# Optimization experiments

Measured on AMD Instinct MI355X. Metric: run time of the kernel, lower is better.

The kernel has to match this reference:

```python
import jax, jax.numpy as jnp
import numpy as np

N_HEAD = 16

def setup_inputs() -> dict:
    key = jax.random.key(0)
    ks = jax.random.split(key, 5)
    C = 1024
    x = jax.random.normal(ks[0], (2, 2048, C), dtype=jnp.float32)
    w_attn = jax.random.normal(ks[1], (C, 3 * C), dtype=jnp.float32) * (C ** -0.5)
    b_attn = jax.random.normal(ks[2], (3 * C,), dtype=jnp.float32) * 0.02
    w_proj = jax.random.normal(ks[3], (C, C), dtype=jnp.float32) * (C ** -0.5)
    b_proj = jax.random.normal(ks[4], (C,), dtype=jnp.float32) * 0.02
    return {"x": x, "w_attn": w_attn, "b_attn": b_attn, "w_proj": w_proj, "b_proj": b_proj}

def reference(x, w_attn, b_attn, w_proj, b_proj):
    B, T, C = x.shape
    H = N_HEAD
    D = C // H  # head_dim
    qkv = x @ w_attn + b_attn  # [B,T,3C]
    q, k, v = jnp.split(qkv, 3, axis=-1)
    # [B,T,H,D] -> [B,H,T,D]
    q = q.reshape(B, T, H, D).transpose(0, 2, 1, 3)
    k = k.reshape(B, T, H, D).transpose(0, 2, 1, 3)
    v = v.reshape(B, T, H, D).transpose(0, 2, 1, 3)
    scale = 1.0 / np.sqrt(D).astype(np.float32)
    att = jnp.einsum('bhqd,bhkd->bhqk', q, k) * scale  # [B,H,T,T]
    causal = jnp.tril(jnp.ones((T, T), dtype=bool))
    att = jnp.where(causal, att, jnp.finfo(att.dtype).min)
    att = jax.nn.softmax(att, axis=-1)
    y = jnp.einsum('bhqk,bhkd->bhqd', att, v)  # [B,H,T,D]
    y = y.transpose(0, 2, 1, 3).reshape(B, T, C)
    return y @ w_proj + b_proj
```

## Files before the change

kernel.cpp:

```cpp
#include <hip/hip_runtime.h>
#include <hip/hip_bf16.h>
#include <stdint.h>

typedef __bf16 bf16x8 __attribute__((ext_vector_type(8)));
typedef __bf16 bf16x4 __attribute__((ext_vector_type(4)));
typedef float  f32x4  __attribute__((ext_vector_type(4)));

#define GLOBAL_AS __attribute__((address_space(1)))
#define LDS_AS    __attribute__((address_space(3)))

__device__ __forceinline__ void gld_lds16(const __bf16* g, __bf16* l) {
  __builtin_amdgcn_global_load_lds((GLOBAL_AS void*)g, (LDS_AS void*)l, 16, 0, 0);
}

#define QSCALE 0.18033688011116029f

__device__ __forceinline__ unsigned pk2(float a, float b) {
  unsigned short ua = __builtin_bit_cast(unsigned short, (__bf16)a);
  unsigned short ub = __builtin_bit_cast(unsigned short, (__bf16)b);
  return (unsigned)ua | ((unsigned)ub << 16);
}

union PackU { unsigned u[4]; bf16x8 v; };

__global__ __launch_bounds__(256) void cast_bf16_kernel(const float* __restrict__ src,
                                                        __bf16* __restrict__ dst, int n)
{
  int i = (blockIdx.x * 256 + threadIdx.x) * 8;
  if (i >= n) return;
  float4 a = *(const float4*)(src + i);
  float4 b = *(const float4*)(src + i + 4);
  bf16x8 o;
  o[0]=(__bf16)a.x; o[1]=(__bf16)a.y; o[2]=(__bf16)a.z; o[3]=(__bf16)a.w;
  o[4]=(__bf16)b.x; o[5]=(__bf16)b.y; o[6]=(__bf16)b.z; o[7]=(__bf16)b.w;
  *(bf16x8*)(dst + i) = o;
}

__global__ __launch_bounds__(256) void transpose_cast_kernel(const float* __restrict__ src,
                                                             __bf16* __restrict__ dst,
                                                             int R, int C)
{
  __shared__ float tile[32][33];
  int c0 = blockIdx.x * 32, r0 = blockIdx.y * 32;
  int tx = threadIdx.x & 31, ty = threadIdx.x >> 5;
  #pragma unroll
  for (int i = 0; i < 32; i += 8)
    tile[ty + i][tx] = src[(size_t)(r0 + ty + i) * C + (c0 + tx)];
  __syncthreads();
  #pragma unroll
  for (int i = 0; i < 32; i += 8)
    dst[(size_t)(c0 + ty + i) * R + (r0 + tx)] = (__bf16)tile[tx][ty + i];
}

template<int MODE, int BM>
__global__ __launch_bounds__(256, (BM == 128 ? 3 : 2))
void gemm_kernel(const __bf16* __restrict__ A,
                 const __bf16* __restrict__ Bt,
                 const float*  __restrict__ bias,
                 float* __restrict__ outF,
                 __bf16* __restrict__ qb,
                 __bf16* __restrict__ kb,
                 __bf16* __restrict__ vb,
                 int M, int N, int K)
{
  __shared__ __bf16 As[BM * 64];
  __shared__ __bf16 Bs[128 * 64];
  const int tid  = threadIdx.x;
  const int wave = tid >> 6, lane = tid & 63;
  const int lo = lane & 15, g4 = lane >> 4;
  int bm, bn;
  if (MODE == 0) {
    int bid = blockIdx.x;
    int bm_i = (bid & 7) * 4 + ((bid >> 3) & 3);
    int bn_i = bid >> 5;
    bm = bm_i * 128; bn = bn_i * 128;
  } else {
    bm = blockIdx.y * BM; bn = blockIdx.x * 128;
  }
  const int wr = (wave >> 1) * (BM / 2);
  const int wc = (wave & 1) * 64;
  constexpr int MF = BM / 32;

  f32x4 acc[MF][4] = {};

  const int nkt = K >> 6;
  for (int kt = 0; kt < nkt; ++kt) {
    const int k0 = kt << 6;
    __syncthreads();
    #pragma unroll
    for (int j = 0; j < BM / 32; ++j) {
      int c = j * 256 + tid;
      int r = c >> 3, cc = c & 7;
      int cs = cc ^ (r & 7);
      gld_lds16(A + (size_t)(bm + r) * K + (k0 + cs * 8), As + c * 8);
    }
    #pragma unroll
    for (int j = 0; j < 4; ++j) {
      int c = j * 256 + tid;
      int r = c >> 3, cc = c & 7;
      int cs = cc ^ (r & 7);
      gld_lds16(Bt + (size_t)(bn + r) * K + (k0 + cs * 8), Bs + c * 8);
    }
    __syncthreads();
    #pragma unroll
    for (int ks = 0; ks < 2; ++ks) {
      bf16x8 af[MF], bfr[4];
      #pragma unroll
      for (int mf = 0; mf < MF; ++mf) {
        int row = wr + mf * 16 + lo;
        int ch = (ks * 4 + g4) ^ (row & 7);
        af[mf] = *(const bf16x8*)(As + row * 64 + ch * 8);
      }
      #pragma unroll
      for (int nf = 0; nf < 4; ++nf) {
        int row = wc + nf * 16 + lo;
        int ch = (ks * 4 + g4) ^ (row & 7);
        bfr[nf] = *(const bf16x8*)(Bs + row * 64 + ch * 8);
      }
      #pragma unroll
      for (int mf = 0; mf < MF; ++mf)
        #pragma unroll
        for (int nf = 0; nf < 4; ++nf)
          acc[mf][nf] = __builtin_amdgcn_mfma_f32_16x16x32_bf16(af[mf], bfr[nf], acc[mf][nf], 0, 0, 0);
    }
  }

  float bv[4];
  #pragma unroll
  for (int nf = 0; nf < 4; ++nf) bv[nf] = bias[bn + wc + nf * 16 + lo];

  if (MODE == 1) {
    #pragma unroll
    for (int mf = 0; mf < MF; ++mf)
      #pragma unroll
      for (int nf = 0; nf < 4; ++nf) {
        int col = bn + wc + nf * 16 + lo;
        #pragma unroll
        for (int j = 0; j < 4; ++j) {
          int row = bm + wr + mf * 16 + g4 * 4 + j;
          outF[(size_t)row * N + col] = acc[mf][nf][j] + bv[nf];
        }
      }
  } else {
    #pragma unroll
    for (int mf = 0; mf < MF; ++mf) {
      const int tbase = bm + wr + mf * 16 + g4 * 4;
      const int b = tbase >> 11, t = tbase & 2047;
      #pragma unroll
      for (int nf = 0; nf < 4; ++nf) {
        int n = bn + wc + nf * 16 + lo;
        int sel = n >> 10, hd = n & 1023;
        int h = hd >> 6, d = hd & 63;
        size_t bh = (size_t)(b * 16 + h);
        if (sel == 2) {
          bf16x4 pv;
          #pragma unroll
          for (int j = 0; j < 4; ++j) pv[j] = (__bf16)(acc[mf][nf][j] + bv[nf]);
          *(bf16x4*)(vb + (bh * 64 + d) * 2048 + t) = pv;
        } else if (sel == 0) {
          #pragma unroll
          for (int j = 0; j < 4; ++j)
            qb[(bh * 2048 + (size_t)(t + j)) * 64 + d] = (__bf16)((acc[mf][nf][j] + bv[nf]) * QSCALE);
        } else {
          #pragma unroll
          for (int j = 0; j < 4; ++j)
            kb[(bh * 2048 + (size_t)(t + j)) * 64 + d] = (__bf16)(acc[mf][nf][j] + bv[nf]);
        }
      }
    }
  }
}

__global__ __launch_bounds__(256, 4)
void attn_kernel(const __bf16* __restrict__ qg_, const __bf16* __restrict__ kg,
                 const __bf16* __restrict__ vg, __bf16* __restrict__ yg,
                 __bf16* __restrict__ pY, float* __restrict__ pL)
{
  const int n = blockIdx.x;
  const int xcd = n & 7;
  const int m = n >> 3;
  const int bh = xcd + 8 * (m & 3);
  const int t = m >> 2;
  const int b = bh >> 4, h = bh & 15;

  const int tid  = threadIdx.x;
  const int wave = tid >> 6;
  const int lane = tid & 63;
  const int l15  = lane & 15;
  const int g    = lane >> 4;
  const int sw   = l15 & 7;

  __shared__ __bf16 Kb[2][64 * 64];
  __shared__ __bf16 Vb[2][64 * 64];

  const __bf16* qbase = qg_ + (size_t)bh * 2048 * 64;
  const __bf16* kbase = kg  + (size_t)bh * 2048 * 64;
  const __bf16* vbase = vg  + (size_t)bh * 64 * 2048;

  bf16x8 qf0, qf1;
  f32x4 o0, o1, o2, o3, osum;

  bf16x8 ones;
  #pragma unroll
  for (int j = 0; j < 8; ++j) ones[j] = (__bf16)1.0f;

  auto LOADQ = [&](int strip) {
    const int q16 = strip * 64 + wave * 16 + l15;
    qf0 = *(const bf16x8*)(qbase + (size_t)q16 * 64 + g * 8);
    qf1 = *(const bf16x8*)(qbase + (size_t)q16 * 64 + 32 + g * 8);
  };
  auto RESET = [&]() {
    o0 = f32x4{}; o1 = f32x4{}; o2 = f32x4{}; o3 = f32x4{}; osum = f32x4{};
  };
  auto STAGE = [&](int kt, int bsel) {
    #pragma unroll
    for (int j = 0; j < 2; ++j) {
      int c = j * 256 + tid;
      int cr = c >> 3, cc = c & 7;
      int cs = cc ^ (cr & 7);
      int pr = (cr & 0x23) | ((cr & 0x10) >> 2) | ((cr & 0x0C) << 1);
      gld_lds16(kbase + (size_t)(kt * 64 + pr) * 64 + cs * 8, &Kb[bsel][0] + c * 8);
      gld_lds16(vbase + (size_t)cr * 2048 + (kt * 64 + cs * 8), &Vb[bsel][0] + c * 8);
    }
  };

  auto TILE = [&](int cur, bool diag) {
    const __bf16* KL = &Kb[cur][0];
    f32x4 s0 = {}, s1 = {}, s2 = {}, s3 = {};
    {
      bf16x8 k00 = *(const bf16x8*)(KL + (0  + l15) * 64 + ((0 + g) ^ sw) * 8);
      bf16x8 k01 = *(const bf16x8*)(KL + (0  + l15) * 64 + ((4 + g) ^ sw) * 8);
      s0 = __builtin_amdgcn_mfma_f32_16x16x32_bf16(k00, qf0, s0, 0, 0, 0);
      s0 = __builtin_amdgcn_mfma_f32_16x16x32_bf16(k01, qf1, s0, 0, 0, 0);
      bf16x8 k10 = *(const bf16x8*)(KL + (16 + l15) * 64 + ((0 + g) ^ sw) * 8);
      bf16x8 k11 = *(const bf16x8*)(KL + (16 + l15) * 64 + ((4 + g) ^ sw) * 8);
      s1 = __builtin_amdgcn_mfma_f32_16x16x32_bf16(k10, qf0, s1, 0, 0, 0);
      s1 = __builtin_amdgcn_mfma_f32_16x16x32_bf16(k11, qf1, s1, 0, 0, 0);
      bf16x8 k20 = *(const bf16x8*)(KL + (32 + l15) * 64 + ((0 + g) ^ sw) * 8);
      bf16x8 k21 = *(const bf16x8*)(KL + (32 + l15) * 64 + ((4 + g) ^ sw) * 8);
      s2 = __builtin_amdgcn_mfma_f32_16x16x32_bf16(k20, qf0, s2, 0, 0, 0);
      s2 = __builtin_amdgcn_mfma_f32_16x16x32_bf16(k21, qf1, s2, 0, 0, 0);
      bf16x8 k30 = *(const bf16x8*)(KL + (48 + l15) * 64 + ((0 + g) ^ sw) * 8);
      bf16x8 k31 = *(const bf16x8*)(KL + (48 + l15) * 64 + ((4 + g) ^ sw) * 8);
      s3 = __builtin_amdgcn_mfma_f32_16x16x32_bf16(k30, qf0, s3, 0, 0, 0);
      s3 = __builtin_amdgcn_mfma_f32_16x16x32_bf16(k31, qf1, s3, 0, 0, 0);
    }

    if (diag) {
      const int qr = wave * 16 + l15;
      #pragma unroll
      for (int r2 = 0; r2 < 4; ++r2) {
        if (8 * g + r2          > qr) s0[r2] = -3.0e38f;
        if (8 * g + 4 + r2      > qr) s1[r2] = -3.0e38f;
        if (32 + 8 * g + r2     > qr) s2[r2] = -3.0e38f;
        if (32 + 8 * g + 4 + r2 > qr) s3[r2] = -3.0e38f;
      }
    }

    #pragma unroll
    for (int r2 = 0; r2 < 4; ++r2) s0[r2] = exp2f(s0[r2]);
    #pragma unroll
    for (int r2 = 0; r2 < 4; ++r2) s1[r2] = exp2f(s1[r2]);
    #pragma unroll
    for (int r2 = 0; r2 < 4; ++r2) s2[r2] = exp2f(s2[r2]);
    #pragma unroll
    for (int r2 = 0; r2 < 4; ++r2) s3[r2] = exp2f(s3[r2]);

    PackU pa0, pa1;
    pa0.u[0] = pk2(s0[0], s0[1]); pa0.u[1] = pk2(s0[2], s0[3]);
    pa0.u[2] = pk2(s1[0], s1[1]); pa0.u[3] = pk2(s1[2], s1[3]);
    pa1.u[0] = pk2(s2[0], s2[1]); pa1.u[1] = pk2(s2[2], s2[3]);
    pa1.u[2] = pk2(s3[0], s3[1]); pa1.u[3] = pk2(s3[2], s3[3]);

    osum = __builtin_amdgcn_mfma_f32_16x16x32_bf16(pa0.v, ones, osum, 0, 0, 0);
    osum = __builtin_amdgcn_mfma_f32_16x16x32_bf16(pa1.v, ones, osum, 0, 0, 0);

    const __bf16* VL = &Vb[cur][0];
    {
      bf16x8 v00 = *(const bf16x8*)(VL + (0  + l15) * 64 + ((0 + g) ^ sw) * 8);
      bf16x8 v01 = *(const bf16x8*)(VL + (0  + l15) * 64 + ((4 + g) ^ sw) * 8);
      o0 = __builtin_amdgcn_mfma_f32_16x16x32_bf16(pa0.v, v00, o0, 0, 0, 0);
      o0 = __builtin_amdgcn_mfma_f32_16x16x32_bf16(pa1.v, v01, o0, 0, 0, 0);
      bf16x8 v10 = *(const bf16x8*)(VL + (16 + l15) * 64 + ((0 + g) ^ sw) * 8);
      bf16x8 v11 = *(const bf16x8*)(VL + (16 + l15) * 64 + ((4 + g) ^ sw) * 8);
      o1 = __builtin_amdgcn_mfma_f32_16x16x32_bf16(pa0.v, v10, o1, 0, 0, 0);
      o1 = __builtin_amdgcn_mfma_f32_16x16x32_bf16(pa1.v, v11, o1, 0, 0, 0);
      bf16x8 v20 = *(const bf16x8*)(VL + (32 + l15) * 64 + ((0 + g) ^ sw) * 8);
      bf16x8 v21 = *(const bf16x8*)(VL + (32 + l15) * 64 + ((4 + g) ^ sw) * 8);
      o2 = __builtin_amdgcn_mfma_f32_16x16x32_bf16(pa0.v, v20, o2, 0, 0, 0);
      o2 = __builtin_amdgcn_mfma_f32_16x16x32_bf16(pa1.v, v21, o2, 0, 0, 0);
      bf16x8 v30 = *(const bf16x8*)(VL + (48 + l15) * 64 + ((0 + g) ^ sw) * 8);
      bf16x8 v31 = *(const bf16x8*)(VL + (48 + l15) * 64 + ((4 + g) ^ sw) * 8);
      o3 = __builtin_amdgcn_mfma_f32_16x16x32_bf16(pa0.v, v30, o3, 0, 0, 0);
      o3 = __builtin_amdgcn_mfma_f32_16x16x32_bf16(pa1.v, v31, o3, 0, 0, 0);
    }
  };

  auto WRITE_Y = [&](int strip) {
    #pragma unroll
    for (int r2 = 0; r2 < 4; ++r2) {
      float il = 1.0f / osum[r2];
      int trow = strip * 64 + wave * 16 + 4 * g + r2;
      __bf16* dst = yg + ((size_t)(b * 2048 + trow)) * 1024 + h * 64;
      dst[l15]      = (__bf16)(o0[r2] * il);
      dst[16 + l15] = (__bf16)(o1[r2] * il);
      dst[32 + l15] = (__bf16)(o2[r2] * il);
      dst[48 + l15] = (__bf16)(o3[r2] * il);
    }
  };
  auto WRITE_PART = [&](int slot) {
    __bf16* po = pY + (size_t)slot * 4096;
    #pragma unroll
    for (int r2 = 0; r2 < 4; ++r2) {
      int row = wave * 16 + 4 * g + r2;
      __bf16* dst = po + row * 64;
      dst[l15]      = (__bf16)o0[r2];
      dst[16 + l15] = (__bf16)o1[r2];
      dst[32 + l15] = (__bf16)o2[r2];
      dst[48 + l15] = (__bf16)o3[r2];
    }
    if (l15 == 0) {
      #pragma unroll
      for (int r2 = 0; r2 < 4; ++r2)
        pL[slot * 64 + wave * 16 + 4 * g + r2] = osum[r2];
    }
  };

  int cur = 0;
  if (t < 16) {
    LOADQ(t); RESET();
    STAGE(0, 0);
    for (int j = 0; j < 17; ++j) {
      __syncthreads();
      if (j < 16) {
        int nx = j + 1;
        STAGE((nx <= t) ? nx : (nx + 15 - t), cur ^ 1);
      }
      if (j <= t) {
        TILE(cur, j == t);
        if (j == t) { WRITE_Y(t); LOADQ(31 - t); RESET(); }
      } else {
        TILE(cur, j == 16);
      }
      cur ^= 1;
    }
    WRITE_PART((bh * 16 + (15 - t)) * 2 + 1);
  } else {
    LOADQ(t); RESET();
    STAGE(0, 0);
    for (int j = 0; j < 16; ++j) {
      __syncthreads();
      if (j < 15) STAGE(j + 1, cur ^ 1);
      TILE(cur, false);
      cur ^= 1;
    }
    WRITE_PART((bh * 16 + (t - 16)) * 2);
  }
}

__global__ __launch_bounds__(256)
void attn_merge_kernel(const __bf16* __restrict__ pY, const float* __restrict__ pL,
                       __bf16* __restrict__ yg)
{
  const int us = blockIdx.x & 15, bh = blockIdx.x >> 4;
  const int b = bh >> 4, h = bh & 15;
  const int tid = threadIdx.x;
  const int row = tid >> 2, d0 = (tid & 3) * 16;
  const int slotA = (bh * 16 + us) * 2, slotB = slotA + 1;

  float l = pL[slotA * 64 + row] + pL[slotB * 64 + row];
  float inv = 1.0f / l;

  const __bf16* pa = pY + (size_t)slotA * 4096 + row * 64 + d0;
  const __bf16* pb = pY + (size_t)slotB * 4096 + row * 64 + d0;
  __bf16* dst = yg + ((size_t)(b * 2048 + (16 + us) * 64 + row)) * 1024 + h * 64 + d0;

  bf16x8 a0 = *(const bf16x8*)pa, a1 = *(const bf16x8*)(pa + 8);
  bf16x8 b0 = *(const bf16x8*)pb, b1 = *(const bf16x8*)(pb + 8);
  bf16x8 r0, r1;
  #pragma unroll
  for (int j = 0; j < 8; ++j) {
    r0[j] = (__bf16)(((float)a0[j] + (float)b0[j]) * inv);
    r1[j] = (__bf16)(((float)a1[j] + (float)b1[j]) * inv);
  }
  *(bf16x8*)dst = r0;
  *(bf16x8*)(dst + 8) = r1;
}

extern "C" void kernel_launch(void* const* d_in, const int* in_sizes, int n_in,
                              void* d_out, int out_size, void* d_ws, size_t ws_size,
                              hipStream_t stream)
{
  const float* x      = (const float*)d_in[0];
  const float* w_attn = (const float*)d_in[1];
  const float* b_attn = (const float*)d_in[2];
  const float* w_proj = (const float*)d_in[3];
  const float* b_proj = (const float*)d_in[4];
  float* out = (float*)d_out;

  __bf16* xb  = (__bf16*)d_ws;
  __bf16* waT = xb  + (size_t)4096 * 1024;
  __bf16* wpT = waT + (size_t)3072 * 1024;
  __bf16* qb  = wpT + (size_t)1024 * 1024;
  __bf16* kb  = qb  + (size_t)32 * 2048 * 64;
  __bf16* vb  = kb  + (size_t)32 * 2048 * 64;
  __bf16* yb  = vb  + (size_t)32 * 2048 * 64;

  __bf16* pY = xb;
  float*  pL = (float*)waT;

  cast_bf16_kernel<<<2048, 256, 0, stream>>>(x, xb, 4096 * 1024);
  transpose_cast_kernel<<<dim3(96, 32), 256, 0, stream>>>(w_attn, waT, 1024, 3072);
  transpose_cast_kernel<<<dim3(32, 32), 256, 0, stream>>>(w_proj, wpT, 1024, 1024);
  gemm_kernel<0, 128><<<768, 256, 0, stream>>>(xb, waT, b_attn, nullptr,
                                               qb, kb, vb, 4096, 3072, 1024);
  attn_kernel<<<1024, 256, 0, stream>>>(qb, kb, vb, yb, pY, pL);
  attn_merge_kernel<<<512, 256, 0, stream>>>(pY, pL, yb);
  gemm_kernel<1, 64><<<dim3(8, 64), 256, 0, stream>>>(yb, wpT, b_proj, out,
                                                      nullptr, nullptr, nullptr, 4096, 1024, 1024);
}
```

Before: 99.80 us.

## Restructure attention into single-wave blocks with 32-key tiles and no barriers

After: 111.7 us. 12.0% more time.

```diff
diff --git a/kernel.cpp b/kernel.cpp
--- a/kernel.cpp
+++ b/kernel.cpp
@@ -171,209 +171,213 @@
   }
 }
 
-__global__ __launch_bounds__(256, 4)
-void attn_kernel(const __bf16* __restrict__ qg_, const __bf16* __restrict__ kg,
+__global__ __launch_bounds__(64, 2)
+void attn_kernel(const __bf16* __restrict__ qg, const __bf16* __restrict__ kg,
                  const __bf16* __restrict__ vg, __bf16* __restrict__ yg,
                  __bf16* __restrict__ pY, float* __restrict__ pL)
 {
   const int n = blockIdx.x;
   const int xcd = n & 7;
-  const int m = n >> 3;
-  const int bh = xcd + 8 * (m & 3);
-  const int t = m >> 2;
+  const int w = n >> 3;
+  const int bh = xcd + 8 * (w & 3);
+  const int c = w >> 2;
   const int b = bh >> 4, h = bh & 15;
 
-  const int tid  = threadIdx.x;
-  const int wave = tid >> 6;
-  const int lane = tid & 63;
-  const int l15  = lane & 15;
-  const int g    = lane >> 4;
-  const int sw   = l15 & 7;
-
-  __shared__ __bf16 Kb[2][64 * 64];
-  __shared__ __bf16 Vb[2][64 * 64];
-
-  const __bf16* qbase = qg_ + (size_t)bh * 2048 * 64;
-  const __bf16* kbase = kg  + (size_t)bh * 2048 * 64;
-  const __bf16* vbase = vg  + (size_t)bh * 64 * 2048;
-
-  bf16x8 qf0, qf1;
-  f32x4 o0, o1, o2, o3, osum;
+  const int lane = threadIdx.x;
+  const int l15 = lane & 15, g = lane >> 4;
+
+  __shared__ __bf16 KV[2][4096];
+
+  const __bf16* qbase = qg + (size_t)bh * 2048 * 64;
+  const __bf16* kbase = kg + (size_t)bh * 2048 * 64;
+  const __bf16* vbase = vg + (size_t)bh * 64 * 2048;
+
+  bf16x8 qf[2][2];
+  f32x4 o[2][4], osum[2];
 
   bf16x8 ones;
   #pragma unroll
   for (int j = 0; j < 8; ++j) ones[j] = (__bf16)1.0f;
 
   auto LOADQ = [&](int strip) {
-    const int q16 = strip * 64 + wave * 16 + l15;
-    qf0 = *(const bf16x8*)(qbase + (size_t)q16 * 64 + g * 8);
-    qf1 = *(const bf16x8*)(qbase + (size_t)q16 * 64 + 32 + g * 8);
+    #pragma unroll
+    for (int sub = 0; sub < 2; ++sub) {
+      const int q16 = strip * 32 + sub * 16 + l15;
+      qf[sub][0] = *(const bf16x8*)(qbase + (size_t)q16 * 64 + g * 8);
+      qf[sub][1] = *(const bf16x8*)(qbase + (size_t)q16 * 64 + 32 + g * 8);
+    }
   };
   auto RESET = [&]() {
-    o0 = f32x4{}; o1 = f32x4{}; o2 = f32x4{}; o3 = f32x4{}; osum = f32x4{};
+    #pragma unroll
+    for (int sub = 0; sub < 2; ++sub) {
+      #pragma unroll
+      for (int nb = 0; nb < 4; ++nb) o[sub][nb] = f32x4{};
+      osum[sub] = f32x4{};
+    }
   };
   auto STAGE = [&](int kt, int bsel) {
-    #pragma unroll
-    for (int j = 0; j < 2; ++j) {
-      int c = j * 256 + tid;
-      int cr = c >> 3, cc = c & 7;
-      int cs = cc ^ (cr & 7);
-      int pr = (cr & 0x23) | ((cr & 0x10) >> 2) | ((cr & 0x0C) << 1);
-      gld_lds16(kbase + (size_t)(kt * 64 + pr) * 64 + cs * 8, &Kb[bsel][0] + c * 8);
-      gld_lds16(vbase + (size_t)cr * 2048 + (kt * 64 + cs * 8), &Vb[bsel][0] + c * 8);
+    __bf16* KD = &KV[bsel][0];
+    __bf16* VD = &KV[bsel][2048];
+    #pragma unroll
+    for (int j = 0; j < 4; ++j) {
+      int cc = j * 64 + lane;
+      int mu = cc >> 3, sl = cc & 7;
+      int pr = (mu & 3) | ((mu & 0x0C) << 1) | ((mu & 0x10) >> 2);
+      gld_lds16(kbase + (size_t)(kt * 32 + pr) * 64 + ((sl ^ (mu & 7)) * 8), KD + cc * 8);
+    }
+    #pragma unroll
+    for (int j = 0; j < 4; ++j) {
+      int cc = j * 64 + lane;
+      int d = cc >> 2, sl = cc & 3;
+      gld_lds16(vbase + (size_t)d * 2048 + kt * 32 + ((sl ^ ((d >> 1) & 3)) * 8), VD + cc * 8);
     }
   };
 
   auto TILE = [&](int cur, bool diag) {
-    const __bf16* KL = &Kb[cur][0];
-    f32x4 s0 = {}, s1 = {}, s2 = {}, s3 = {};
-    {
-      bf16x8 k00 = *(const bf16x8*)(KL + (0  + l15) * 64 + ((0 + g) ^ sw) * 8);
-      bf16x8 k01 = *(const bf16x8*)(KL + (0  + l15) * 64 + ((4 + g) ^ sw) * 8);
-      s0 = __builtin_amdgcn_mfma_f32_16x16x32_bf16(k00, qf0, s0, 0, 0, 0);
-      s0 = __builtin_amdgcn_mfma_f32_16x16x32_bf16(k01, qf1, s0, 0, 0, 0);
-      bf16x8 k10 = *(const bf16x8*)(KL + (16 + l15) * 64 + ((0 + g) ^ sw) * 8);
-      bf16x8 k11 = *(const bf16x8*)(KL + (16 + l15) * 64 + ((4 + g) ^ sw) * 8);
-      s1 = __builtin_amdgcn_mfma_f32_16x16x32_bf16(k10, qf0, s1, 0, 0, 0);
-      s1 = __builtin_amdgcn_mfma_f32_16x16x32_bf16(k11, qf1, s1, 0, 0, 0);
-      bf16x8 k20 = *(const bf16x8*)(KL + (32 + l15) * 64 + ((0 + g) ^ sw) * 8);
-      bf16x8 k21 = *(const bf16x8*)(KL + (32 + l15) * 64 + ((4 + g) ^ sw) * 8);
-      s2 = __builtin_amdgcn_mfma_f32_16x16x32_bf16(k20, qf0, s2, 0, 0, 0);
-      s2 = __builtin_amdgcn_mfma_f32_16x16x32_bf16(k21, qf1, s2, 0, 0, 0);
-      bf16x8 k30 = *(const bf16x8*)(KL + (48 + l15) * 64 + ((0 + g) ^ sw) * 8);
-      bf16x8 k31 = *(const bf16x8*)(KL + (48 + l15) * 64 + ((4 + g) ^ sw) * 8);
-      s3 = __builtin_amdgcn_mfma_f32_16x16x32_bf16(k30, qf0, s3, 0, 0, 0);
-      s3 = __builtin_amdgcn_mfma_f32_16x16x32_bf16(k31, qf1, s3, 0, 0, 0);
-    }
+    const __bf16* KL = &KV[cur][0];
+    const __bf16* VL = &KV[cur][2048];
+    bf16x8 kf[2][2];
+    #pragma unroll
+    for (int mb = 0; mb < 2; ++mb)
+      #pragma unroll
+      for (int ks = 0; ks < 2; ++ks)
+        kf[mb][ks] = *(const bf16x8*)(KL + (mb * 16 + l15) * 64 + (((ks * 4 + g) ^ (l15 & 7)) * 8));
+
+    f32x4 s[2][2] = {};
+    #pragma unroll
+    for (int sub = 0; sub < 2; ++sub)
+      #pragma unroll
+      for (int mb = 0; mb < 2; ++mb) {
+        s[sub][mb] = __builtin_amdgcn_mfma_f32_16x16x32_bf16(kf[mb][0], qf[sub][0], s[sub][mb], 0, 0, 0);
+        s[sub][mb] = __builtin_amdgcn_mfma_f32_16x16x32_bf16(kf[mb][1], qf[sub][1], s[sub][mb], 0, 0, 0);
+      }
 
     if (diag) {
-      const int qr = wave * 16 + l15;
+      #pragma unroll
+      for (int sub = 0; sub < 2; ++sub) {
+        const int qr = sub * 16 + l15;
+        #pragma unroll
+        for (int mb = 0; mb < 2; ++mb)
+          #pragma unroll
+          for (int r2 = 0; r2 < 4; ++r2)
+            if (8 * g + 4 * mb + r2 > qr) s[sub][mb][r2] = -3.0e38f;
+      }
+    }
+
+    #pragma unroll
+    for (int sub = 0; sub < 2; ++sub)
+      #pragma unroll
+      for (int mb = 0; mb < 2; ++mb)
+        #pragma unroll
+        for (int r2 = 0; r2 < 4; ++r2)
+          s[sub][mb][r2] = exp2f(s[sub][mb][r2]);
+
+    PackU pa[2];
+    #pragma unroll
+    for (int sub = 0; sub < 2; ++sub) {
+      pa[sub].u[0] = pk2(s[sub][0][0], s[sub][0][1]);
+      pa[sub].u[1] = pk2(s[sub][0][2], s[sub][0][3]);
+      pa[sub].u[2] = pk2(s[sub][1][0], s[sub][1][1]);
+      pa[sub].u[3] = pk2(s[sub][1][2], s[sub][1][3]);
+    }
+
+    osum[0] = __builtin_amdgcn_mfma_f32_16x16x32_bf16(pa[0].v, ones, osum[0], 0, 0, 0);
+    osum[1] = __builtin_amdgcn_mfma_f32_16x16x32_bf16(pa[1].v, ones, osum[1], 0, 0, 0);
+
+    #pragma unroll
+    for (int nb = 0; nb < 4; ++nb) {
+      bf16x8 vf = *(const bf16x8*)(VL + (nb * 16 + l15) * 32 + ((g ^ ((l15 >> 1) & 3)) * 8));
+      o[0][nb] = __builtin_amdgcn_mfma_f32_16x16x32_bf16(pa[0].v, vf, o[0][nb], 0, 0, 0);
+      o[1][nb] = __builtin_amdgcn_mfma_f32_16x16x32_bf16(pa[1].v, vf, o[1][nb], 0, 0, 0);
+    }
+  };
+
+  auto WRITE_Y = [&](int strip) {
+    #pragma unroll
+    for (int sub = 0; sub < 2; ++sub)
       #pragma unroll
       for (int r2 = 0; r2 < 4; ++r2) {
-        if (8 * g + r2          > qr) s0[r2] = -3.0e38f;
-        if (8 * g + 4 + r2      > qr) s1[r2] = -3.0e38f;
-        if (32 + 8 * g + r2     > qr) s2[r2] = -3.0e38f;
-        if (32 + 8 * g + 4 + r2 > qr) s3[r2] = -3.0e38f;
-      }
-    }
-
-    #pragma unroll
-    for (int r2 = 0; r2 < 4; ++r2) s0[r2] = exp2f(s0[r2]);
-    #pragma unroll
-    for (int r2 = 0; r2 < 4; ++r2) s1[r2] = exp2f(s1[r2]);
-    #pragma unroll
-    for (int r2 = 0; r2 < 4; ++r2) s2[r2] = exp2f(s2[r2]);
-    #pragma unroll
-    for (int r2 = 0; r2 < 4; ++r2) s3[r2] = exp2f(s3[r2]);
-
-    PackU pa0, pa1;
-    pa0.u[0] = pk2(s0[0], s0[1]); pa0.u[1] = pk2(s0[2], s0[3]);
-    pa0.u[2] = pk2(s1[0], s1[1]); pa0.u[3] = pk2(s1[2], s1[3]);
-    pa1.u[0] = pk2(s2[0], s2[1]); pa1.u[1] = pk2(s2[2], s2[3]);
-    pa1.u[2] = pk2(s3[0], s3[1]); pa1.u[3] = pk2(s3[2], s3[3]);
-
-    osum = __builtin_amdgcn_mfma_f32_16x16x32_bf16(pa0.v, ones, osum, 0, 0, 0);
-    osum = __builtin_amdgcn_mfma_f32_16x16x32_bf16(pa1.v, ones, osum, 0, 0, 0);
-
-    const __bf16* VL = &Vb[cur][0];
-    {
-      bf16x8 v00 = *(const bf16x8*)(VL + (0  + l15) * 64 + ((0 + g) ^ sw) * 8);
-      bf16x8 v01 = *(const bf16x8*)(VL + (0  + l15) * 64 + ((4 + g) ^ sw) * 8);
-      o0 = __builtin_amdgcn_mfma_f32_16x16x32_bf16(pa0.v, v00, o0, 0, 0, 0);
-      o0 = __builtin_amdgcn_mfma_f32_16x16x32_bf16(pa1.v, v01, o0, 0, 0, 0);
-      bf16x8 v10 = *(const bf16x8*)(VL + (16 + l15) * 64 + ((0 + g) ^ sw) * 8);
-      bf16x8 v11 = *(const bf16x8*)(VL + (16 + l15) * 64 + ((4 + g) ^ sw) * 8);
-      o1 = __builtin_amdgcn_mfma_f32_16x16x32_bf16(pa0.v, v10, o1, 0, 0, 0);
-      o1 = __builtin_amdgcn_mfma_f32_16x16x32_bf16(pa1.v, v11, o1, 0, 0, 0);
-      bf16x8 v20 = *(const bf16x8*)(VL + (32 + l15) * 64 + ((0 + g) ^ sw) * 8);
-      bf16x8 v21 = *(const bf16x8*)(VL + (32 + l15) * 64 + ((4 + g) ^ sw) * 8);
-      o2 = __builtin_amdgcn_mfma_f32_16x16x32_bf16(pa0.v, v20, o2, 0, 0, 0);
-      o2 = __builtin_amdgcn_mfma_f32_16x16x32_bf16(pa1.v, v21, o2, 0, 0, 0);
-      bf16x8 v30 = *(const bf16x8*)(VL + (48 + l15) * 64 + ((0 + g) ^ sw) * 8);
-      bf16x8 v31 = *(const bf16x8*)(VL + (48 + l15) * 64 + ((4 + g) ^ sw) * 8);
-      o3 = __builtin_amdgcn_mfma_f32_16x16x32_bf16(pa0.v, v30, o3, 0, 0, 0);
-      o3 = __builtin_amdgcn_mfma_f32_16x16x32_bf16(pa1.v, v31, o3, 0, 0, 0);
-    }
-  };
-
-  auto WRITE_Y = [&](int strip) {
-    #pragma unroll
-    for (int r2 = 0; r2 < 4; ++r2) {
-      float il = 1.0f / osum[r2];
-      int trow = strip * 64 + wave * 16 + 4 * g + r2;
-      __bf16* dst = yg + ((size_t)(b * 2048 + trow)) * 1024 + h * 64;
-      dst[l15]      = (__bf16)(o0[r2] * il);
-      dst[16 + l15] = (__bf16)(o1[r2] * il);
-      dst[32 + l15] = (__bf16)(o2[r2] * il);
-      dst[48 + l15] = (__bf16)(o3[r2] * il);
-    }
+        float il = 1.0f / osum[sub][r2];
+        int trow = strip * 32 + sub * 16 + 4 * g + r2;
+        __bf16* dst = yg + ((size_t)(b * 2048 + trow)) * 1024 + h * 64;
+        dst[l15]      = (__bf16)(o[sub][0][r2] * il);
+        dst[16 + l15] = (__bf16)(o[sub][1][r2] * il);
+        dst[32 + l15] = (__bf16)(o[sub][2][r2] * il);
+        dst[48 + l15] = (__bf16)(o[sub][3][r2] * il);
+      }
   };
   auto WRITE_PART = [&](int slot) {
-    __bf16* po = pY + (size_t)slot * 4096;
-    #pragma unroll
-    for (int r2 = 0; r2 < 4; ++r2) {
-      int row = wave * 16 + 4 * g + r2;
-      __bf16* dst = po + row * 64;
-      dst[l15]      = (__bf16)o0[r2];
-      dst[16 + l15] = (__bf16)o1[r2];
-      dst[32 + l15] = (__bf16)o2[r2];
-      dst[48 + l15] = (__bf16)o3[r2];
-    }
+    __bf16* po = pY + (size_t)slot * 2048;
+    #pragma unroll
+    for (int sub = 0; sub < 2; ++sub)
+      #pragma unroll
+      for (int r2 = 0; r2 < 4; ++r2) {
+        int row = sub * 16 + 4 * g + r2;
+        __bf16* dst = po + row * 64;
+        dst[l15]      = (__bf16)o[sub][0][r2];
+        dst[16 + l15] = (__bf16)o[sub][1][r2];
+        dst[32 + l15] = (__bf16)o[sub][2][r2];
+        dst[48 + l15] = (__bf16)o[sub][3][r2];
+      }
     if (l15 == 0) {
       #pragma unroll
-      for (int r2 = 0; r2 < 4; ++r2)
-        pL[slot * 64 + wave * 16 + 4 * g + r2] = osum[r2];
+      for (int sub = 0; sub < 2; ++sub)
+        #pragma unroll
+        for (int r2 = 0; r2 < 4; ++r2)
+          pL[slot * 32 + sub * 16 + 4 * g + r2] = osum[sub][r2];
     }
   };
 
   int cur = 0;
-  if (t < 16) {
-    LOADQ(t); RESET();
+  if (c < 32) {
+    auto kvn = [&](int j) { return (j <= c) ? j : (j + 31 - c); };
+    LOADQ(c); RESET();
+    STAGE(kvn(0), 0);
+    for (int j = 0; j < 33; ++j) {
+      if (j < 32) {
+        STAGE(kvn(j + 1), cur ^ 1);
+        asm volatile("s_waitcnt vmcnt(8)" ::: "memory");
+      } else {
+        asm volatile("s_waitcnt vmcnt(0)" ::: "memory");
+      }
+      TILE(cur, (j == c) || (j == 32));
+      if (j == c) { WRITE_Y(c); LOADQ(63 - c); RESET(); }
+      cur ^= 1;
+    }
+    WRITE_PART((bh * 32 + (31 - c)) * 2 + 1);
+  } else {
+    LOADQ(c); RESET();
     STAGE(0, 0);
-    for (int j = 0; j < 17; ++j) {
-      __syncthreads();
-      if (j < 16) {
-        int nx = j + 1;
-        STAGE((nx <= t) ? nx : (nx + 15 - t), cur ^ 1);
-      }
-      if (j <= t) {
-        TILE(cur, j == t);
-        if (j == t) { WRITE_Y(t); LOADQ(31 - t); RESET(); }
+    for (int j = 0; j < 32; ++j) {
+      if (j < 31) {
+        STAGE(j + 1, cur ^ 1);
+        asm volatile("s_waitcnt vmcnt(8)" ::: "memory");
       } else {
-        TILE(cur, j == 16);
-      }
-      cur ^= 1;
-    }
-    WRITE_PART((bh * 16 + (15 - t)) * 2 + 1);
-  } else {
-    LOADQ(t); RESET();
-    STAGE(0, 0);
-    for (int j = 0; j < 16; ++j) {
-      __syncthreads();
-      if (j < 15) STAGE(j + 1, cur ^ 1);
+        asm volatile("s_waitcnt vmcnt(0)" ::: "memory");
+      }
       TILE(cur, false);
       cur ^= 1;
     }
-    WRITE_PART((bh * 16 + (t - 16)) * 2);
+    WRITE_PART((bh * 32 + (c - 32)) * 2);
   }
 }
 
-__global__ __launch_bounds__(256)
+__global__ __launch_bounds__(128)
 void attn_merge_kernel(const __bf16* __restrict__ pY, const float* __restrict__ pL,
                        __bf16* __restrict__ yg)
 {
-  const int us = blockIdx.x & 15, bh = blockIdx.x >> 4;
+  const int us = blockIdx.x & 31, bh = blockIdx.x >> 5;
   const int b = bh >> 4, h = bh & 15;
-  const int tid = threadIdx.x;
-  const int row = tid >> 2, d0 = (tid & 3) * 16;
-  const int slotA = (bh * 16 + us) * 2, slotB = slotA + 1;
-
-  float l = pL[slotA * 64 + row] + pL[slotB * 64 + row];
+  const int row = threadIdx.x >> 2, d0 = (threadIdx.x & 3) * 16;
+  const int slotA = (bh * 32 + us) * 2, slotB = slotA + 1;
+
+  float l = pL[slotA * 32 + row] + pL[slotB * 32 + row];
   float inv = 1.0f / l;
 
-  const __bf16* pa = pY + (size_t)slotA * 4096 + row * 64 + d0;
-  const __bf16* pb = pY + (size_t)slotB * 4096 + row * 64 + d0;
-  __bf16* dst = yg + ((size_t)(b * 2048 + (16 + us) * 64 + row)) * 1024 + h * 64 + d0;
+  const __bf16* pa = pY + (size_t)slotA * 2048 + row * 64 + d0;
+  const __bf16* pb = pY + (size_t)slotB * 2048 + row * 64 + d0;
+  int trow = (32 + us) * 32 + row;
+  __bf16* dst = yg + ((size_t)(b * 2048 + trow)) * 1024 + h * 64 + d0;
 
   bf16x8 a0 = *(const bf16x8*)pa, a1 = *(const bf16x8*)(pa + 8);
   bf16x8 b0 = *(const bf16x8*)pb, b1 = *(const bf16x8*)(pb + 8);
@@ -414,8 +418,8 @@
   transpose_cast_kernel<<<dim3(32, 32), 256, 0, stream>>>(w_proj, wpT, 1024, 1024);
   gemm_kernel<0, 128><<<768, 256, 0, stream>>>(xb, waT, b_attn, nullptr,
                                                qb, kb, vb, 4096, 3072, 1024);
-  attn_kernel<<<1024, 256, 0, stream>>>(qb, kb, vb, yb, pY, pL);
-  attn_merge_kernel<<<512, 256, 0, stream>>>(pY, pL, yb);
+  attn_kernel<<<2048, 64, 0, stream>>>(qb, kb, vb, yb, pY, pL);
+  attn_merge_kernel<<<1024, 128, 0, stream>>>(pY, pL, yb);
   gemm_kernel<1, 64><<<dim3(8, 64), 256, 0, stream>>>(yb, wpT, b_proj, out,
                                                       nullptr, nullptr, nullptr, 4096, 1024, 1024);
 }
```
